# Optimization experiments

Hardware: AMD Instinct MI355X
Metric: run time of the kernel (lower is better)

Reference implementation:

```python
import jax, jax.numpy as jnp
import numpy as np

N_NODES = 50000
N_EDGES = 640000
D = 128
BN_EPS = 1e-5


def setup_inputs() -> dict:
    key = jax.random.key(0)
    k1, k2, k3 = jax.random.split(key, 3)
    x = jax.random.normal(k1, (N_NODES, D), dtype=jnp.float32)
    # Glorot-ish weight for GCNConv linear
    W = jax.random.normal(k2, (D, D), dtype=jnp.float32) * (1.0 / np.sqrt(D))
    b = jnp.zeros((D,), dtype=jnp.float32)
    gamma = jnp.ones((D,), dtype=jnp.float32)
    beta = jnp.zeros((D,), dtype=jnp.float32)
    edge_index = jax.random.randint(k3, (2, N_EDGES), 0, N_NODES, dtype=jnp.int64)
    return {"x": x, "W": W, "b": b, "gamma": gamma, "beta": beta, "edge_index": edge_index}


def reference(x, W, b, gamma, beta, edge_index):
    N = x.shape[0]
    # --- GCNConv: x' = D^{-1/2} (A + I) D^{-1/2} (x W) + b ---
    xw = x @ W  # [N, D]
    loops = jnp.arange(N, dtype=edge_index.dtype)
    src = jnp.concatenate([edge_index[0], loops])  # [E+N]
    dst = jnp.concatenate([edge_index[1], loops])
    ones = jnp.ones(src.shape[0], dtype=x.dtype)
    deg = jax.ops.segment_sum(ones, dst, num_segments=N)  # in-degree incl. self-loop
    dinv = jnp.where(deg > 0, jax.lax.rsqrt(deg), 0.0)
    norm = dinv[src] * dinv[dst]  # [E+N]
    msg = xw[src] * norm[:, None]  # [E+N, D] gathered + scaled messages
    h = jax.ops.segment_sum(msg, dst, num_segments=N) + b  # scatter-add aggregation
    # --- BatchNorm1d (training-mode batch stats over nodes, biased var) ---
    mean = jnp.mean(h, axis=0)
    var = jnp.mean(jnp.square(h - mean), axis=0)
    h = (h - mean) * jax.lax.rsqrt(var + BN_EPS) * gamma + beta
    # --- activation (relu) ---
    h = jax.nn.relu(h)
    # --- residual (in_channels == out_channels) ---
    h = x + h
    # --- dropout: identity in eval mode for deterministic reference ---
    return h
```

## Files before the change

kernel.cpp:

```cpp
#include <hip/hip_runtime.h>

#define DCH 128
#define ROWS 16
#define BN_EPS 1e-5f

typedef unsigned short u16;
typedef __attribute__((ext_vector_type(8))) short short8;
typedef __attribute__((ext_vector_type(4))) float floatx4;

__device__ __forceinline__ float bf2f(u16 u) {
    return __uint_as_float(((unsigned)u) << 16);
}
__device__ __forceinline__ u16 f2bf(float f) {
    unsigned u = __float_as_uint(f);
    u += 0x7FFFu + ((u >> 16) & 1u);
    return (u16)(u >> 16);
}
__device__ __forceinline__ float ldf(const void* p, int i, int isbf) {
    return isbf ? bf2f(((const u16*)p)[i]) : ((const float*)p)[i];
}

__global__ void prep_kernel(const int* ei, int ewords, const u16* xw, int* ws_i,
                            const void* W, u16* Wb, float* zbase, int zn) {
    int t = threadIdx.x;
    if (blockIdx.x == 0) {
        __shared__ int s_nz, s_hits;
        if (t == 0) { s_nz = 0; s_hits = 0; }
        __syncthreads();
        int nz = 0;
        for (int i = t; i < 1024; i += 256) {
            int w = 2 * i + 1;
            if (w < ewords) nz |= ei[w];
        }
        if (nz) atomicOr(&s_nz, 1);
        unsigned m = (xw[2 * t] >> 8) & 0x7F;
        if (m >= 0x3B && m <= 0x43) atomicAdd(&s_hits, 1);
        __syncthreads();
        int isbf = (s_hits >= 128) ? 1 : 0;
        if (t == 0) {
            ws_i[0] = (s_nz == 0) ? 1 : 0;
            ws_i[1] = isbf;
            ws_i[2] = 0;
        }
        for (int idx = t; idx < DCH * DCH; idx += 256) {
            int j = idx & 7, lane = (idx >> 3) & 63, kk = (idx >> 9) & 3, nt = idx >> 11;
            int k = kk * 32 + (lane >> 4) * 8 + j;
            int n = nt * 16 + (lane & 15);
            Wb[idx] = f2bf(ldf(W, k * DCH + n, isbf));
        }
    } else {
        int stride = (gridDim.x - 1) * 256;
        for (int i = (blockIdx.x - 1) * 256 + t; i < zn; i += stride) zbase[i] = 0.f;
    }
}

__global__ void zero_kernel(float* p, int n) {
    int stride = gridDim.x * 256;
    for (int i = blockIdx.x * 256 + threadIdx.x; i < n; i += stride) p[i] = 0.f;
}

__global__ void paint_kernel(u16* out, int n, unsigned val) {
    int stride = gridDim.x * 256;
    for (int i = blockIdx.x * 256 + threadIdx.x; i < n; i += stride) out[i] = (u16)val;
}

__global__ void detect_kernel(const int* ei, int ewords, const u16* xw, int* ws_i) {
    __shared__ int s_nz, s_hits;
    int t = threadIdx.x;
    if (t == 0) { s_nz = 0; s_hits = 0; }
    __syncthreads();
    int nz = 0;
    for (int i = t; i < 1024; i += 256) {
        int w = 2 * i + 1;
        if (w < ewords) nz |= ei[w];
    }
    if (nz) atomicOr(&s_nz, 1);
    unsigned m = (xw[2 * t] >> 8) & 0x7F;
    if (m >= 0x3B && m <= 0x43) atomicAdd(&s_hits, 1);
    __syncthreads();
    if (t == 0) {
        ws_i[0] = (s_nz == 0) ? 1 : 0;
        ws_i[1] = (s_hits >= 128) ? 1 : 0;
        ws_i[2] = 0;
    }
}

__global__ void deg_kernel(const int* ei, int E, int* ws_i, int* deg, int N) {
    int is64 = ws_i[0];
    int i = blockIdx.x * 256 + threadIdx.x;
    if (i < E) {
        int s = is64 ? ei[2 * i] : ei[i];
        int d = is64 ? ei[2 * E + 2 * i] : ei[E + i];
        if (((unsigned)s >= (unsigned)N) || ((unsigned)d >= (unsigned)N))
            atomicOr(&ws_i[2], 2);
        d = min(max(d, 0), N - 1);
        atomicAdd(&deg[d], 1);
    }
}

__global__ void dinv_kernel(const int* deg, float* dinv, int N, int* ws_i) {
    int i = blockIdx.x * 256 + threadIdx.x;
    if (i < N) {
        float v = rsqrtf((float)(deg[i] + 1));
        if (!(v > 0.f && v <= 1.001f)) atomicOr(&ws_i[2], 4);
        dinv[i] = v;
    }
}

__global__ void scanA_kernel(const int* deg, int* part, int N) {
    int base = blockIdx.x * 1024 + threadIdx.x * 4;
    int s = 0;
    #pragma unroll
    for (int j = 0; j < 4; ++j) {
        int i = base + j;
        if (i < N) s += deg[i];
    }
    #pragma unroll
    for (int o = 1; o < 64; o <<= 1) s += __shfl_xor(s, o, 64);
    __shared__ int ws4[4];
    if ((threadIdx.x & 63) == 0) ws4[threadIdx.x >> 6] = s;
    __syncthreads();
    if (threadIdx.x == 0) part[blockIdx.x] = ws4[0] + ws4[1] + ws4[2] + ws4[3];
}

__global__ void scanB_kernel(int* part, int P) {
    __shared__ int wsum[4];
    int t = threadIdx.x, lane = t & 63, w = t >> 6;
    int v = (t < P) ? part[t] : 0;
    int sc = v;
    #pragma unroll
    for (int o = 1; o < 64; o <<= 1) {
        int u = __shfl_up(sc, o, 64);
        if (lane >= o) sc += u;
    }
    if (lane == 63) wsum[w] = sc;
    __syncthreads();
    if (t < 4) {
        int s = wsum[t];
        #pragma unroll
        for (int o = 1; o < 4; o <<= 1) {
            int u = __shfl_up(s, o, 4);
            if (t >= o) s += u;
        }
        wsum[t] = s;
    }
    __syncthreads();
    int excl = sc - v + (w ? wsum[w - 1] : 0);
    if (t < P) part[t] = excl;
}

__global__ void scanC_kernel(int* deg_cursor, const int* part, int* rowptr,
                             float* dinv, int N) {
    __shared__ int wsum[4];
    int t = threadIdx.x, lane = t & 63, w = t >> 6;
    int base = blockIdx.x * 1024 + t * 4;
    int v[4], ts = 0;
    #pragma unroll
    for (int j = 0; j < 4; ++j) {
        int i = base + j;
        v[j] = (i < N) ? deg_cursor[i] : 0;
        ts += v[j];
    }
    int sc = ts;
    #pragma unroll
    for (int o = 1; o < 64; o <<= 1) {
        int u = __shfl_up(sc, o, 64);
        if (lane >= o) sc += u;
    }
    if (lane == 63) wsum[w] = sc;
    __syncthreads();
    if (t < 4) {
        int s = wsum[t];
        #pragma unroll
        for (int o = 1; o < 4; o <<= 1) {
            int u = __shfl_up(s, o, 4);
            if (t >= o) s += u;
        }
        wsum[t] = s;
    }
    __syncthreads();
    int run = sc - ts + (w ? wsum[w - 1] : 0) + part[blockIdx.x];
    #pragma unroll
    for (int j = 0; j < 4; ++j) {
        int i = base + j;
        if (i < N) {
            deg_cursor[i] = run;
            run += v[j];
            rowptr[i + 1] = run;
            dinv[i] = rsqrtf((float)(v[j] + 1));
        }
    }
    if (blockIdx.x == 0 && t == 0) rowptr[0] = 0;
}

__global__ void fillcsr_kernel(const int* ei, int E, const int* ws_i,
                               int* cursor, int* col, int N) {
    int is64 = ws_i[0];
    int i = blockIdx.x * 256 + threadIdx.x;
    if (i < E) {
        int s = is64 ? ei[2 * i] : ei[i];
        int d = is64 ? ei[2 * E + 2 * i] : ei[E + i];
        s = min(max(s, 0), N - 1);
        d = min(max(d, 0), N - 1);
        int pos = atomicAdd(&cursor[d], 1);
        col[pos] = s;
    }
}

__global__ void gemm_mfma_kernel(const void* x, const u16* Wb, const float* dinv,
                                 const int* ws_i, u16* y, int N) {
    int isbf = ws_i[1];
    int t = threadIdx.x;
    int wv = t >> 6, lane = t & 63;
    int quad = lane >> 4, l16 = lane & 15;
    int r0 = blockIdx.x * 64 + wv * 16;
    int rl = min(r0 + l16, N - 1);
    short8 a[4];
    if (isbf) {
        const u16* xp = (const u16*)x + (size_t)rl * DCH + quad * 8;
        #pragma unroll
        for (int kk = 0; kk < 4; ++kk)
            a[kk] = *(const short8*)(xp + kk * 32);
    } else {
        const float* xp = (const float*)x + (size_t)rl * DCH + quad * 8;
        #pragma unroll
        for (int kk = 0; kk < 4; ++kk) {
            float4 f0 = *(const float4*)(xp + kk * 32);
            float4 f1 = *(const float4*)(xp + kk * 32 + 4);
            short8 aa;
            aa[0] = (short)f2bf(f0.x); aa[1] = (short)f2bf(f0.y);
            aa[2] = (short)f2bf(f0.z); aa[3] = (short)f2bf(f0.w);
            aa[4] = (short)f2bf(f1.x); aa[5] = (short)f2bf(f1.y);
            aa[6] = (short)f2bf(f1.z); aa[7] = (short)f2bf(f1.w);
            a[kk] = aa;
        }
    }
    floatx4 acc[8];
    #pragma unroll
    for (int i = 0; i < 8; ++i) acc[i] = (floatx4)(0.f);
    #pragma unroll
    for (int nt = 0; nt < 8; ++nt) {
        #pragma unroll
        for (int kk = 0; kk < 4; ++kk) {
            short8 bfr = *(const short8*)&Wb[(((nt << 2) | kk) * 64 + lane) * 8];
            acc[nt] = __builtin_amdgcn_mfma_f32_16x16x32_bf16(a[kk], bfr, acc[nt], 0, 0, 0);
        }
    }
    #pragma unroll
    for (int i = 0; i < 4; ++i) {
        int row = r0 + quad * 4 + i;
        if (row < N) {
            float dv = dinv[row];
            #pragma unroll
            for (int nt = 0; nt < 8; ++nt)
                y[(size_t)row * DCH + nt * 16 + l16] = f2bf(acc[nt][i] * dv);
        }
    }
}

__global__ void gather_stats_kernel(const int* rowptr, const int* col, const u16* y,
                                    const float* dinv, const void* b, const int* ws_i,
                                    float* h, float* sums, float* sumsq, int N) {
    int isbf = ws_i[1];
    int t = threadIdx.x;
    int w = t >> 6, lane = t & 63;
    int g = lane >> 4, cl = lane & 15;
    int c0 = cl * 8;
    float bb[8];
    #pragma unroll
    for (int k = 0; k < 8; ++k) bb[k] = ldf(b, c0 + k, isbf);
    float ps[8], pq[8];
    #pragma unroll
    for (int k = 0; k < 8; ++k) { ps[k] = 0.f; pq[k] = 0.f; }
    int wid = blockIdx.x * 4 + w;
    int nw = gridDim.x * 4;
    for (int n = wid; n < N; n += nw) {
        float acc[8];
        if (g == 0) {
            uint4 q = *(const uint4*)&y[(size_t)n * DCH + c0];
            acc[0] = bf2f((u16)(q.x & 0xFFFF)); acc[1] = bf2f((u16)(q.x >> 16));
            acc[2] = bf2f((u16)(q.y & 0xFFFF)); acc[3] = bf2f((u16)(q.y >> 16));
            acc[4] = bf2f((u16)(q.z & 0xFFFF)); acc[5] = bf2f((u16)(q.z >> 16));
            acc[6] = bf2f((u16)(q.w & 0xFFFF)); acc[7] = bf2f((u16)(q.w >> 16));
        } else {
            #pragma unroll
            for (int k = 0; k < 8; ++k) acc[k] = 0.f;
        }
        int beg = rowptr[n], end = rowptr[n + 1];
        for (int j = beg + g; j < end; j += 4) {
            int s = col[j];
            uint4 q = *(const uint4*)&y[(size_t)s * DCH + c0];
            acc[0] += bf2f((u16)(q.x & 0xFFFF)); acc[1] += bf2f((u16)(q.x >> 16));
            acc[2] += bf2f((u16)(q.y & 0xFFFF)); acc[3] += bf2f((u16)(q.y >> 16));
            acc[4] += bf2f((u16)(q.z & 0xFFFF)); acc[5] += bf2f((u16)(q.z >> 16));
            acc[6] += bf2f((u16)(q.w & 0xFFFF)); acc[7] += bf2f((u16)(q.w >> 16));
        }
        #pragma unroll
        for (int k = 0; k < 8; ++k) {
            acc[k] += __shfl_xor(acc[k], 16, 64);
            acc[k] += __shfl_xor(acc[k], 32, 64);
        }
        if (g == 0) {
            float dn = dinv[n];
            float4 o0, o1;
            o0.x = fmaf(acc[0], dn, bb[0]); o0.y = fmaf(acc[1], dn, bb[1]);
            o0.z = fmaf(acc[2], dn, bb[2]); o0.w = fmaf(acc[3], dn, bb[3]);
            o1.x = fmaf(acc[4], dn, bb[4]); o1.y = fmaf(acc[5], dn, bb[5]);
            o1.z = fmaf(acc[6], dn, bb[6]); o1.w = fmaf(acc[7], dn, bb[7]);
            float* hp = &h[(size_t)n * DCH + c0];
            *(float4*)hp = o0;
            *(float4*)(hp + 4) = o1;
            ps[0] += o0.x; pq[0] += o0.x * o0.x;
            ps[1] += o0.y; pq[1] += o0.y * o0.y;
            ps[2] += o0.z; pq[2] += o0.z * o0.z;
            ps[3] += o0.w; pq[3] += o0.w * o0.w;
            ps[4] += o1.x; pq[4] += o1.x * o1.x;
            ps[5] += o1.y; pq[5] += o1.y * o1.y;
            ps[6] += o1.z; pq[6] += o1.z * o1.z;
            ps[7] += o1.w; pq[7] += o1.w * o1.w;
        }
    }
    __shared__ float lps[4][DCH], lpq[4][DCH];
    if (g == 0) {
        #pragma unroll
        for (int k = 0; k < 8; ++k) { lps[w][c0 + k] = ps[k]; lpq[w][c0 + k] = pq[k]; }
    }
    __syncthreads();
    if (t < DCH) {
        float s = (lps[0][t] + lps[1][t]) + (lps[2][t] + lps[3][t]);
        float q = (lpq[0][t] + lpq[1][t]) + (lpq[2][t] + lpq[3][t]);
        atomicAdd(&sums[t], s);
        atomicAdd(&sumsq[t], q);
    }
}

__global__ void gemm_valu_kernel(const void* x, const void* W, const float* dinv,
                                 const int* ws_i, void* y, int N) {
    __shared__ float WsF[64 * DCH];
    __shared__ float xs[ROWS * DCH];
    int isbf = ws_i[1];
    int t = threadIdx.x;
    int r0 = blockIdx.x * ROWS;
    for (int i = t; i < ROWS * DCH; i += 256) {
        int r = r0 + (i >> 7);
        xs[i] = (r < N) ? ldf(x, r * DCH + (i & 127), isbf) : 0.f;
    }
    int d = t & 127, rh = t >> 7;
    float s[8];
    #pragma unroll
    for (int j = 0; j < 8; ++j) s[j] = 0.f;
    for (int half = 0; half < 2; ++half) {
        __syncthreads();
        for (int i = t; i < 64 * DCH; i += 256)
            WsF[i] = ldf(W, half * 64 * DCH + i, isbf);
        __syncthreads();
        #pragma unroll
        for (int j = 0; j < 8; ++j) {
            int rr = rh + 2 * j;
            float a = s[j];
            #pragma unroll 16
            for (int k = 0; k < 64; ++k)
                a = fmaf(xs[rr * DCH + half * 64 + k], WsF[k * DCH + d], a);
            s[j] = a;
        }
    }
    #pragma unroll
    for (int j = 0; j < 8; ++j) {
        int r = r0 + rh + 2 * j;
        if (r < N) {
            float v = s[j] * dinv[r];
            if (isbf) ((u16*)y)[r * DCH + d] = f2bf(v);
            else      ((float*)y)[r * DCH + d] = v;
        }
    }
}

__global__ void scatter_kernel(const int* ei, int E, const int* ws_i,
                               const void* y, float* acc, int N) {
    int is64 = ws_i[0], isbf = ws_i[1];
    int gid = blockIdx.x * 256 + threadIdx.x;
    int e = gid >> 5;
    if (e >= E) return;
    int c0 = (gid & 31) * 4;
    int s = is64 ? ei[2 * e] : ei[e];
    int d = is64 ? ei[2 * E + 2 * e] : ei[E + e];
    s = min(max(s, 0), N - 1);
    d = min(max(d, 0), N - 1);
    float v0, v1, v2, v3;
    if (isbf) {
        uint2 raw = *(const uint2*)&((const u16*)y)[s * DCH + c0];
        v0 = bf2f((u16)(raw.x & 0xFFFF)); v1 = bf2f((u16)(raw.x >> 16));
        v2 = bf2f((u16)(raw.y & 0xFFFF)); v3 = bf2f((u16)(raw.y >> 16));
    } else {
        float4 raw = *(const float4*)&((const float*)y)[s * DCH + c0];
        v0 = raw.x; v1 = raw.y; v2 = raw.z; v3 = raw.w;
    }
    float* a = &acc[d * DCH + c0];
    atomicAdd(a + 0, v0);
    atomicAdd(a + 1, v1);
    atomicAdd(a + 2, v2);
    atomicAdd(a + 3, v3);
}

__global__ void bnstat_kernel(const void* y, float* acc, const float* dinv,
                              const void* b, int* ws_i,
                              float* sums, float* sumsq, int total) {
    int isbf = ws_i[1];
    int t = threadIdx.x;
    int d = t & 127;
    float bb = ldf(b, d, isbf);
    float ps = 0.f, pq = 0.f;
    int stride = gridDim.x * 256;
    for (int i = blockIdx.x * 256 + t; i < total; i += stride) {
        int r = i >> 7;
        float yv = isbf ? bf2f(((const u16*)y)[i]) : ((const float*)y)[i];
        float v = (yv + acc[i]) * dinv[r] + bb;
        acc[i] = v;
        ps += v;
        pq += v * v;
    }
    __shared__ float ls[256], lq[256];
    ls[t] = ps; lq[t] = pq;
    __syncthreads();
    if (t < 128) {
        atomicAdd(&sums[d], ls[t] + ls[t + 128]);
        atomicAdd(&sumsq[d], lq[t] + lq[t + 128]);
    }
}

__global__ void out_kernel(const float* h, const void* x,
                           const void* gamma, const void* beta,
                           int* ws_i, const float* sums, const float* sumsq,
                           void* out, int total, float invN) {
    __shared__ float sc[DCH], sh[DCH];
    int isbf = ws_i[1];
    int t = threadIdx.x;
    if (t < DCH) {
        float mean = sums[t] * invN;
        float var = fmaxf(sumsq[t] * invN - mean * mean, 0.f);
        float s = ldf(gamma, t, isbf) * rsqrtf(var + BN_EPS);
        if (!(var < 1e8f && fabsf(s) < 1e6f)) atomicOr(&ws_i[2], 32);
        sc[t] = s;
        sh[t] = ldf(beta, t, isbf) - mean * s;
    }
    __syncthreads();
    int stride = gridDim.x * 256;
    if (isbf) {
        for (int i = blockIdx.x * 256 + t; i < total; i += stride) {
            int d = i & 127;
            float v = fmaf(h[i], sc[d], sh[d]);
            v = fmaxf(v, 0.f) + bf2f(((const u16*)x)[i]);
            ((u16*)out)[i] = f2bf(v);
        }
    } else {
        for (int i = blockIdx.x * 256 + t; i < total; i += stride) {
            int d = i & 127;
            float v = fmaf(h[i], sc[d], sh[d]);
            v = fmaxf(v, 0.f) + ((const float*)x)[i];
            ((float*)out)[i] = v;
        }
    }
}

__global__ void diag_kernel(const int* ws_i, void* out, int n) {
    int e = ws_i[2];
    if (!e) return;
    int isbf = ws_i[1];
    float v = 4096.f + 32.f * (float)(e & 63);
    int stride = gridDim.x * 256;
    if (isbf) {
        u16 code = f2bf(v);
        for (int i = blockIdx.x * 256 + threadIdx.x; i < n; i += stride)
            ((u16*)out)[i] = code;
    } else {
        for (int i = blockIdx.x * 256 + threadIdx.x; i < n; i += stride)
            ((float*)out)[i] = v;
    }
}

extern "C" void kernel_launch(void* const* d_in, const int* in_sizes, int n_in,
                              void* d_out, int out_size, void* d_ws, size_t ws_size,
                              hipStream_t stream) {
    const void* x     = d_in[0];
    const void* W     = d_in[1];
    const void* b     = d_in[2];
    const void* gamma = d_in[3];
    const void* beta  = d_in[4];
    const int*  ei    = (const int*)d_in[5];

    const int N  = in_sizes[0] / DCH;
    const int E  = in_sizes[5] / 2;
    const int ND = N * DCH;
    const int P  = (N + 1023) / 1024;

    char* wsb = (char*)d_ws;
    int*  ws_i = (int*)wsb;

    size_t o_wb   = 64;
    size_t o_deg  = o_wb + 32768;
    size_t o_sum  = o_deg + 4 * (size_t)N;
    size_t o_sq   = o_sum + 512;
    size_t o_rp   = o_sq + 512;
    size_t o_dinv = o_rp + 4 * ((size_t)N + 1) + 4;
    size_t o_part = o_dinv + 4 * (size_t)N;
    size_t o_h    = (o_part + 1024 + 255) & ~(size_t)255;
    size_t o_col  = o_h + 4 * (size_t)ND;
    size_t need_csr = o_col + 4 * (size_t)E;

    (void)hipGetLastError();

    if (ws_size >= need_csr) {
        u16*   Wb    = (u16*)(wsb + o_wb);
        int*   deg   = (int*)(wsb + o_deg);
        float* sums  = (float*)(wsb + o_sum);
        float* sumsq = (float*)(wsb + o_sq);
        int*   rowptr= (int*)(wsb + o_rp);
        float* dinv  = (float*)(wsb + o_dinv);
        int*   part  = (int*)(wsb + o_part);
        float* h     = (float*)(wsb + o_h);
        int*   col   = (int*)(wsb + o_col);
        u16*   y     = (u16*)d_out;

        prep_kernel<<<65, 256, 0, stream>>>(ei, 2 * E, (const u16*)x, ws_i,
                                            W, Wb, (float*)(wsb + o_deg), N + 256);
        deg_kernel<<<(E + 255) / 256, 256, 0, stream>>>(ei, E, ws_i, deg, N);
        scanA_kernel<<<P, 256, 0, stream>>>(deg, part, N);
        scanB_kernel<<<1, 256, 0, stream>>>(part, P);
        scanC_kernel<<<P, 256, 0, stream>>>(deg, part, rowptr, dinv, N);
        fillcsr_kernel<<<(E + 255) / 256, 256, 0, stream>>>(ei, E, ws_i, deg, col, N);
        gemm_mfma_kernel<<<(N + 63) / 64, 256, 0, stream>>>(x, Wb, dinv, ws_i, y, N);
        gather_stats_kernel<<<1024, 256, 0, stream>>>(rowptr, col, y, dinv, b, ws_i,
                                                      h, sums, sumsq, N);
        out_kernel<<<1024, 256, 0, stream>>>(h, x, gamma, beta, ws_i, sums, sumsq,
                                             d_out, ND, 1.0f / (float)N);
        diag_kernel<<<512, 256, 0, stream>>>(ws_i, d_out, out_size);
    } else {
        int*   deg   = (int*)(wsb + 16);
        float* dinv  = (float*)(wsb + 16 + 4 * (size_t)N);
        float* sums  = (float*)(wsb + 16 + 8 * (size_t)N);
        float* sumsq = sums + DCH;
        float* acc   = sumsq + DCH;
        size_t need = 16 + 8 * (size_t)N + 1024 + 4 * (size_t)ND;
        if (ws_size < need) {
            int mb = (int)(ws_size >> 20); if (mb > 127) mb = 127;
            float v = 2048.f + 16.f * (float)mb;
            unsigned u; __builtin_memcpy(&u, &v, 4);
            paint_kernel<<<1024, 256, 0, stream>>>((u16*)d_out, out_size, u >> 16);
            return;
        }
        detect_kernel<<<1, 256, 0, stream>>>(ei, 2 * E, (const u16*)x, ws_i);
        zero_kernel<<<2048, 256, 0, stream>>>((float*)(wsb + 16), 2 * N + 256 + ND);
        deg_kernel<<<(E + 255) / 256, 256, 0, stream>>>(ei, E, ws_i, deg, N);
        dinv_kernel<<<(N + 255) / 256, 256, 0, stream>>>(deg, dinv, N, ws_i);
        gemm_valu_kernel<<<(N + ROWS - 1) / ROWS, 256, 0, stream>>>(x, W, dinv, ws_i, d_out, N);
        scatter_kernel<<<(E * 32 + 255) / 256, 256, 0, stream>>>(ei, E, ws_i, d_out, acc, N);
        bnstat_kernel<<<240, 256, 0, stream>>>(d_out, acc, dinv, b, ws_i, sums, sumsq, ND);
        out_kernel<<<256, 256, 0, stream>>>(acc, x, gamma, beta, ws_i, sums, sumsq,
                                            d_out, ND, 1.0f / (float)N);
        diag_kernel<<<512, 256, 0, stream>>>(ws_i, d_out, out_size);
    }

    if (hipGetLastError() != hipSuccess)
        hipMemsetAsync(d_out, 0x42, (size_t)out_size * 2, stream);
}
```

Baseline: 264.7 us.

## Remap gather-aggregation to half-wave per node with 4-way unrolled neighbor loads

Restructures the gather/stats kernel so each 32-lane half-wave owns one node and handles 4 channels per lane. Neighbors are processed sequentially with a 4-way unrolled loop that has independent accumulators, which removes the cross-lane shuffle reduction and the idle g!=0 lanes during the epilogue. It also staggers the channel order of the final atomics per block to reduce contention on the same addresses. The risk is that 8-byte loads per lane and serial neighbor walks reduce memory-level parallelism for low-degree nodes.

```diff
diff --git a/kernel.cpp b/kernel.cpp
--- a/kernel.cpp
+++ b/kernel.cpp
@@ -263,74 +263,67 @@
                                     float* h, float* sums, float* sumsq, int N) {
     int isbf = ws_i[1];
     int t = threadIdx.x;
-    int w = t >> 6, lane = t & 63;
-    int g = lane >> 4, cl = lane & 15;
-    int c0 = cl * 8;
-    float bb[8];
-    #pragma unroll
-    for (int k = 0; k < 8; ++k) bb[k] = ldf(b, c0 + k, isbf);
-    float ps[8], pq[8];
-    #pragma unroll
-    for (int k = 0; k < 8; ++k) { ps[k] = 0.f; pq[k] = 0.f; }
-    int wid = blockIdx.x * 4 + w;
-    int nw = gridDim.x * 4;
-    for (int n = wid; n < N; n += nw) {
-        float acc[8];
-        if (g == 0) {
-            uint4 q = *(const uint4*)&y[(size_t)n * DCH + c0];
-            acc[0] = bf2f((u16)(q.x & 0xFFFF)); acc[1] = bf2f((u16)(q.x >> 16));
-            acc[2] = bf2f((u16)(q.y & 0xFFFF)); acc[3] = bf2f((u16)(q.y >> 16));
-            acc[4] = bf2f((u16)(q.z & 0xFFFF)); acc[5] = bf2f((u16)(q.z >> 16));
-            acc[6] = bf2f((u16)(q.w & 0xFFFF)); acc[7] = bf2f((u16)(q.w >> 16));
-        } else {
-            #pragma unroll
-            for (int k = 0; k < 8; ++k) acc[k] = 0.f;
-        }
+    int hw = t >> 5;
+    int l32 = t & 31;
+    int c0 = l32 * 4;
+    float bb[4];
+    #pragma unroll
+    for (int k = 0; k < 4; ++k) bb[k] = ldf(b, c0 + k, isbf);
+    float ps[4] = {0.f, 0.f, 0.f, 0.f}, pq[4] = {0.f, 0.f, 0.f, 0.f};
+    int stream_id = blockIdx.x * 8 + hw;
+    int nstreams = gridDim.x * 8;
+    for (int n = stream_id; n < N; n += nstreams) {
+        uint2 qs = *(const uint2*)&y[(size_t)n * DCH + c0];
+        float a0[4] = { bf2f((u16)(qs.x & 0xFFFF)), bf2f((u16)(qs.x >> 16)),
+                        bf2f((u16)(qs.y & 0xFFFF)), bf2f((u16)(qs.y >> 16)) };
+        float a1[4] = {0.f, 0.f, 0.f, 0.f};
+        float a2[4] = {0.f, 0.f, 0.f, 0.f};
+        float a3[4] = {0.f, 0.f, 0.f, 0.f};
         int beg = rowptr[n], end = rowptr[n + 1];
-        for (int j = beg + g; j < end; j += 4) {
-            int s = col[j];
-            uint4 q = *(const uint4*)&y[(size_t)s * DCH + c0];
-            acc[0] += bf2f((u16)(q.x & 0xFFFF)); acc[1] += bf2f((u16)(q.x >> 16));
-            acc[2] += bf2f((u16)(q.y & 0xFFFF)); acc[3] += bf2f((u16)(q.y >> 16));
-            acc[4] += bf2f((u16)(q.z & 0xFFFF)); acc[5] += bf2f((u16)(q.z >> 16));
-            acc[6] += bf2f((u16)(q.w & 0xFFFF)); acc[7] += bf2f((u16)(q.w >> 16));
-        }
-        #pragma unroll
-        for (int k = 0; k < 8; ++k) {
-            acc[k] += __shfl_xor(acc[k], 16, 64);
-            acc[k] += __shfl_xor(acc[k], 32, 64);
-        }
-        if (g == 0) {
-            float dn = dinv[n];
-            float4 o0, o1;
-            o0.x = fmaf(acc[0], dn, bb[0]); o0.y = fmaf(acc[1], dn, bb[1]);
-            o0.z = fmaf(acc[2], dn, bb[2]); o0.w = fmaf(acc[3], dn, bb[3]);
-            o1.x = fmaf(acc[4], dn, bb[4]); o1.y = fmaf(acc[5], dn, bb[5]);
-            o1.z = fmaf(acc[6], dn, bb[6]); o1.w = fmaf(acc[7], dn, bb[7]);
-            float* hp = &h[(size_t)n * DCH + c0];
-            *(float4*)hp = o0;
-            *(float4*)(hp + 4) = o1;
-            ps[0] += o0.x; pq[0] += o0.x * o0.x;
-            ps[1] += o0.y; pq[1] += o0.y * o0.y;
-            ps[2] += o0.z; pq[2] += o0.z * o0.z;
-            ps[3] += o0.w; pq[3] += o0.w * o0.w;
-            ps[4] += o1.x; pq[4] += o1.x * o1.x;
-            ps[5] += o1.y; pq[5] += o1.y * o1.y;
-            ps[6] += o1.z; pq[6] += o1.z * o1.z;
-            ps[7] += o1.w; pq[7] += o1.w * o1.w;
-        }
-    }
-    __shared__ float lps[4][DCH], lpq[4][DCH];
-    if (g == 0) {
-        #pragma unroll
-        for (int k = 0; k < 8; ++k) { lps[w][c0 + k] = ps[k]; lpq[w][c0 + k] = pq[k]; }
-    }
+        int j = beg;
+        for (; j + 3 < end; j += 4) {
+            int s0 = col[j], s1 = col[j + 1], s2 = col[j + 2], s3 = col[j + 3];
+            uint2 q0 = *(const uint2*)&y[(size_t)s0 * DCH + c0];
+            uint2 q1 = *(const uint2*)&y[(size_t)s1 * DCH + c0];
+            uint2 q2 = *(const uint2*)&y[(size_t)s2 * DCH + c0];
+            uint2 q3 = *(const uint2*)&y[(size_t)s3 * DCH + c0];
+            a0[0] += bf2f((u16)(q0.x & 0xFFFF)); a0[1] += bf2f((u16)(q0.x >> 16));
+            a0[2] += bf2f((u16)(q0.y & 0xFFFF)); a0[3] += bf2f((u16)(q0.y >> 16));
+            a1[0] += bf2f((u16)(q1.x & 0xFFFF)); a1[1] += bf2f((u16)(q1.x >> 16));
+            a1[2] += bf2f((u16)(q1.y & 0xFFFF)); a1[3] += bf2f((u16)(q1.y >> 16));
+            a2[0] += bf2f((u16)(q2.x & 0xFFFF)); a2[1] += bf2f((u16)(q2.x >> 16));
+            a2[2] += bf2f((u16)(q2.y & 0xFFFF)); a2[3] += bf2f((u16)(q2.y >> 16));
+            a3[0] += bf2f((u16)(q3.x & 0xFFFF)); a3[1] += bf2f((u16)(q3.x >> 16));
+            a3[2] += bf2f((u16)(q3.y & 0xFFFF)); a3[3] += bf2f((u16)(q3.y >> 16));
+        }
+        for (; j < end; ++j) {
+            uint2 q0 = *(const uint2*)&y[(size_t)col[j] * DCH + c0];
+            a0[0] += bf2f((u16)(q0.x & 0xFFFF)); a0[1] += bf2f((u16)(q0.x >> 16));
+            a0[2] += bf2f((u16)(q0.y & 0xFFFF)); a0[3] += bf2f((u16)(q0.y >> 16));
+        }
+        float dn = dinv[n];
+        float4 o;
+        o.x = fmaf((a0[0] + a1[0]) + (a2[0] + a3[0]), dn, bb[0]);
+        o.y = fmaf((a0[1] + a1[1]) + (a2[1] + a3[1]), dn, bb[1]);
+        o.z = fmaf((a0[2] + a1[2]) + (a2[2] + a3[2]), dn, bb[2]);
+        o.w = fmaf((a0[3] + a1[3]) + (a2[3] + a3[3]), dn, bb[3]);
+        *(float4*)&h[(size_t)n * DCH + c0] = o;
+        ps[0] += o.x; pq[0] += o.x * o.x;
+        ps[1] += o.y; pq[1] += o.y * o.y;
+        ps[2] += o.z; pq[2] += o.z * o.z;
+        ps[3] += o.w; pq[3] += o.w * o.w;
+    }
+    __shared__ float lps[8][DCH], lpq[8][DCH];
+    #pragma unroll
+    for (int k = 0; k < 4; ++k) { lps[hw][c0 + k] = ps[k]; lpq[hw][c0 + k] = pq[k]; }
     __syncthreads();
     if (t < DCH) {
-        float s = (lps[0][t] + lps[1][t]) + (lps[2][t] + lps[3][t]);
-        float q = (lpq[0][t] + lpq[1][t]) + (lpq[2][t] + lpq[3][t]);
-        atomicAdd(&sums[t], s);
-        atomicAdd(&sumsq[t], q);
+        int ch = (t + blockIdx.x * 16) & 127;
+        float s = 0.f, q = 0.f;
+        #pragma unroll
+        for (int i = 0; i < 8; ++i) { s += lps[i][ch]; q += lpq[i][ch]; }
+        atomicAdd(&sums[ch], s);
+        atomicAdd(&sumsq[ch], q);
     }
 }
 
```

New measurement: 251.7 us. -4.9%, faster.
